# Optimization experiments

Measured on AMD Instinct MI355X. Metric: run time of the kernel, lower is better.

Reference implementation:

```python
import jax, jax.numpy as jnp
import numpy as np

N_ATOMS = 4096
HSIZE = 128
N_HEADS = 8
D_K = HSIZE // N_HEADS


def setup_inputs() -> dict:
    key = jax.random.key(0)
    ks = jax.random.split(key, 11)
    s = 1.0 / np.sqrt(HSIZE)
    return {
        "query": jax.random.normal(ks[0], (N_ATOMS, HSIZE), dtype=jnp.float32),
        "key": jax.random.normal(ks[1], (N_ATOMS, HSIZE), dtype=jnp.float32),
        "value": jax.random.normal(ks[2], (N_ATOMS, HSIZE), dtype=jnp.float32),
        "mask": jax.random.randint(ks[3], (N_ATOMS, N_ATOMS), 0, 2, dtype=jnp.int32),
        "Wq": jax.random.normal(ks[4], (HSIZE, HSIZE), dtype=jnp.float32) * s,
        "bq": jnp.zeros((HSIZE,), dtype=jnp.float32),
        "Wk": jax.random.normal(ks[5], (HSIZE, HSIZE), dtype=jnp.float32) * s,
        "bk": jnp.zeros((HSIZE,), dtype=jnp.float32),
        "Wv": jax.random.normal(ks[6], (HSIZE, HSIZE), dtype=jnp.float32) * s,
        "bv": jnp.zeros((HSIZE,), dtype=jnp.float32),
        "Wo": jax.random.normal(ks[7], (HSIZE, HSIZE), dtype=jnp.float32) * s,
    }


def _mha(query, key, value, mask, Wq, bq, Wk, bk, Wv, bv, Wo):
    n = query.shape[0]
    # project and split heads: [n, hsize] -> [H, n, d_k]
    def heads(x, W, b):
        return (x @ W.T + b).reshape(n, N_HEADS, D_K).transpose(1, 0, 2)
    q = heads(query, Wq, bq)
    k = heads(key, Wk, bk)
    v = heads(value, Wv, bv)
    scale = 1.0 / jnp.sqrt(jnp.asarray(D_K, q.dtype))
    scores = jnp.einsum("hnd,hmd->hnm", q, k) * scale  # [H, n, n]
    scores = jnp.where(mask[None, :, :] == 0, jnp.asarray(-1e9, scores.dtype), scores)
    p_attn = jax.nn.softmax(scores, axis=-1)
    x = jnp.einsum("hnm,hmd->hnd", p_attn, v)  # [H, n, d_k]
    x = x.transpose(1, 0, 2).reshape(n, HSIZE)  # merge heads
    return x @ Wo.T  # output_linear has bias=False


def reference(query, key, value, mask, Wq, bq, Wk, bk, Wv, bv, Wo):
    return _mha(query, key, value, mask, Wq, bq, Wk, bk, Wv, bv, Wo)
```

## Files before the change

### kernel.cpp

```cpp
#include <hip/hip_runtime.h>

#define NA 4096
#define HS 128
#define PSTR 72
#define CSTR 136

typedef unsigned short u16;
typedef unsigned long long u64;
using bf16x8  = __attribute__((ext_vector_type(8))) short;
using f32x4   = __attribute__((ext_vector_type(4))) float;
using ushort8 = __attribute__((ext_vector_type(8))) unsigned short;

#define QSCALE 0.18033688011112042f

static __device__ __forceinline__ u16 f2bf(float f) {
    unsigned u = __builtin_bit_cast(unsigned, f);
    u += 0x7FFFu + ((u >> 16) & 1u);
    return (u16)(u >> 16);
}

__global__ __launch_bounds__(256) void cvt_w(
    const float* __restrict__ Wq, const float* __restrict__ Wk,
    const float* __restrict__ Wv, const float* __restrict__ Wo,
    const float* __restrict__ bq, const float* __restrict__ bk,
    const float* __restrict__ bv,
    u16* __restrict__ Wf, float* __restrict__ bb)
{
    const int gid = blockIdx.x * 256 + threadIdx.x;
    const int e = gid * 4;
    const int mat = e >> 14, off = e & 16383;
    const float* src = (mat == 0) ? Wq : (mat == 1) ? Wk : (mat == 2) ? Wv : Wo;
    const float s = (mat == 0) ? QSCALE : 1.0f;
    float4 v = *(const float4*)(src + off);
    ushort4 o;
    o.x = f2bf(v.x * s); o.y = f2bf(v.y * s);
    o.z = f2bf(v.z * s); o.w = f2bf(v.w * s);
    const int j = off >> 7, k0 = off & 127;
    const int j0 = j >> 4, c = j & 15, kk = k0 >> 5, q = (k0 >> 3) & 3;
    const int tgt = mat * 16384 + ((j0 * 4 + kk) * 16 + c) * 32 + q * 8 + (k0 & 7);
    *(ushort4*)(Wf + tgt) = o;
    if (gid < 128)      bb[gid] = bq[gid] * QSCALE;
    else if (gid < 256) bb[gid] = bk[gid - 128];
    else if (gid < 384) bb[gid] = bv[gid - 256];
}

__global__ __launch_bounds__(256) void proj_mfma(
    const float* __restrict__ Xq, const float* __restrict__ Xk, const float* __restrict__ Xv,
    const u16* __restrict__ Wf, const float* __restrict__ bb,
    u16* __restrict__ Qbh, u16* __restrict__ Kbh, u16* __restrict__ VtB)
{
    const int mat = blockIdx.y;
    const float* X = (mat == 0) ? Xq : (mat == 1) ? Xk : Xv;
    const u16* Wm = Wf + mat * 16384;
    const float* bm = bb + mat * 128;
    const int r0b = blockIdx.x * 32;

    __shared__ __align__(16) u16 Xs[32 * CSTR];
    __shared__ __align__(16) u16 Cs[32 * CSTR];

    const int t = threadIdx.x;

    {
        const int r = t >> 3, cb = (t & 7) * 16;
        const float* Xr = X + (size_t)(r0b + r) * HS + cb;
#pragma unroll
        for (int seg = 0; seg < 4; ++seg) {
            float4 f = *(const float4*)(Xr + seg * 4);
            ushort4 u;
            u.x = f2bf(f.x); u.y = f2bf(f.y); u.z = f2bf(f.z); u.w = f2bf(f.w);
            *(ushort4*)(Xs + r * CSTR + cb + seg * 4) = u;
        }
    }
    __syncthreads();

    const int wv = t >> 6, lane = t & 63;
    const int c = lane & 15, q = lane >> 4;
    const int rw = (wv & 1) * 16;
    const int j0b = (wv >> 1) * 4;

    bf16x8 af[4];
#pragma unroll
    for (int kk = 0; kk < 4; ++kk)
        af[kk] = *(const bf16x8*)(Xs + (rw + c) * CSTR + kk * 32 + q * 8);

    const f32x4 zero = {0.f, 0.f, 0.f, 0.f};
#pragma unroll
    for (int jj = 0; jj < 4; ++jj) {
        const int j0 = j0b + jj;
        f32x4 acc = zero;
#pragma unroll
        for (int kk = 0; kk < 4; ++kk) {
            bf16x8 bf = *(const bf16x8*)(Wm + (j0 * 4 + kk) * 512 + c * 32 + q * 8);
            acc = __builtin_amdgcn_mfma_f32_16x16x32_bf16(af[kk], bf, acc, 0, 0, 0);
        }
        const float bias = bm[j0 * 16 + c];
#pragma unroll
        for (int r = 0; r < 4; ++r)
            Cs[(rw + 4 * q + r) * CSTR + j0 * 16 + c] = f2bf(acc[r] + bias);
    }
    __syncthreads();

    if (mat < 2) {
        u16* dst = (mat == 0) ? Qbh : Kbh;
        const int h8 = t >> 5, r = t & 31;
        const u16* src = Cs + r * CSTR + h8 * 16;
        u16* dp = dst + (size_t)h8 * (NA * 16) + (size_t)(r0b + r) * 16;
        *(bf16x8*)(dp)     = *(const bf16x8*)(src);
        *(bf16x8*)(dp + 8) = *(const bf16x8*)(src + 8);
    } else {
        const int d = t >> 1, s = t & 1;
        const int kb = r0b >> 6, ko = (r0b & 32) + s * 16;
        ushort8 v0, v1;
#pragma unroll
        for (int jj = 0; jj < 8; ++jj) v0[jj] = Cs[(s * 16 + jj) * CSTR + d];
#pragma unroll
        for (int jj = 0; jj < 8; ++jj) v1[jj] = Cs[(s * 16 + 8 + jj) * CSTR + d];
        u16* dp = VtB + (size_t)kb * 8192 + d * 64 + ko;
        *(ushort8*)(dp)     = v0;
        *(ushort8*)(dp + 8) = v1;
    }
}

__global__ __launch_bounds__(512, 8) void attn(
    const int* __restrict__ mask,
    const u16* __restrict__ Qbh, const u16* __restrict__ Kbh, const u16* __restrict__ VtB,
    float* __restrict__ part)
{
    __shared__ __align__(16) u16 Pbuf[8 * 16 * PSTR];
    __shared__ __align__(8)  u64 Mwp[16 * 17];

    const int t = threadIdx.x;
    const int h = t >> 6;
    const int lane = t & 63;
    const int c = lane & 15;
    const int q = lane >> 4;
    const int tile = blockIdx.x, split = blockIdx.y;
    const int i0 = tile * 16;
    const int kt0 = split * 1024;

#pragma unroll 4
    for (int rr = 0; rr < 32; ++rr) {
        const int idx = h * 32 + rr;
        const int row = idx >> 4, wc = idx & 15;
        const int v = mask[(size_t)(i0 + row) * NA + kt0 + wc * 64 + lane];
        u64 b = __ballot(v != 0);
        if (lane == 0) Mwp[row * 17 + wc] = b;
    }

    const u16* Qh = Qbh + (size_t)h * (NA * 16);
    const u16* Kh = Kbh + (size_t)h * (NA * 16);

    const bf16x8 qf = *(const bf16x8*)(Qh + (size_t)(i0 + c) * 16 + (q & 1) * 8);

    __syncthreads();

    const f32x4 zero = {0.f, 0.f, 0.f, 0.f};
    f32x4 Oacc = zero;
    float lsum = 0.f;
    u16* Pw = Pbuf + h * 16 * PSTR;

#pragma unroll 1
    for (int it = 0; it < 16; ++it) {
        const int kt = kt0 + it * 64;
        const u16* Vb = VtB + (size_t)(kt >> 6) * 8192 + (h * 16 + c) * 64;

        f32x4 ST[4];
#pragma unroll
        for (int t4 = 0; t4 < 4; ++t4) {
            bf16x8 kf = *(const bf16x8*)(Kh + (size_t)(kt + t4 * 16 + c) * 16 + (q & 1) * 8);
            ST[t4] = __builtin_amdgcn_mfma_f32_16x16x32_bf16(kf, qf, zero, 0, 0, 0);
        }
        bf16x8 vf0 = *(const bf16x8*)(Vb + q * 8);
        bf16x8 vf1 = *(const bf16x8*)(Vb + 32 + q * 8);

        u64 w = Mwp[c * 17 + it] >> (4 * q);
        unsigned mlo = (unsigned)w, mhi = (unsigned)(w >> 32);

#pragma unroll
        for (int t4 = 0; t4 < 4; ++t4) {
            const unsigned mw = (t4 < 2) ? mlo : mhi;
            const int sh = (t4 & 1) * 16;
            float p0 = ((mw >> (sh + 0)) & 1) ? __builtin_amdgcn_exp2f(ST[t4][0]) : 0.f;
            float p1 = ((mw >> (sh + 1)) & 1) ? __builtin_amdgcn_exp2f(ST[t4][1]) : 0.f;
            float p2 = ((mw >> (sh + 2)) & 1) ? __builtin_amdgcn_exp2f(ST[t4][2]) : 0.f;
            float p3 = ((mw >> (sh + 3)) & 1) ? __builtin_amdgcn_exp2f(ST[t4][3]) : 0.f;
            lsum += (p0 + p1) + (p2 + p3);
            unsigned lo = ((__builtin_bit_cast(unsigned, p0) + 0x8000u) >> 16)
                        | ((__builtin_bit_cast(unsigned, p1) + 0x8000u) & 0xFFFF0000u);
            unsigned hi = ((__builtin_bit_cast(unsigned, p2) + 0x8000u) >> 16)
                        | ((__builtin_bit_cast(unsigned, p3) + 0x8000u) & 0xFFFF0000u);
            *(uint2*)(Pw + c * PSTR + t4 * 16 + 4 * q) = make_uint2(lo, hi);
        }
        __asm__ volatile("" ::: "memory");
        __builtin_amdgcn_s_waitcnt(0xC07F);
        __asm__ volatile("" ::: "memory");

        bf16x8 pf0 = *(const bf16x8*)(Pw + c * PSTR + q * 8);
        bf16x8 pf1 = *(const bf16x8*)(Pw + c * PSTR + 32 + q * 8);
        Oacc = __builtin_amdgcn_mfma_f32_16x16x32_bf16(pf0, vf0, Oacc, 0, 0, 0);
        Oacc = __builtin_amdgcn_mfma_f32_16x16x32_bf16(pf1, vf1, Oacc, 0, 0, 0);
    }

    lsum += __shfl_xor(lsum, 16, 64);
    lsum += __shfl_xor(lsum, 32, 64);

    float* base = part + (size_t)((tile * 4 + split) * 8 + h) * 272;
#pragma unroll
    for (int r = 0; r < 4; ++r)
        base[(4 * q + r) * 16 + c] = Oacc[r];
    if (q == 0) base[256 + c] = lsum;
}

__global__ __launch_bounds__(256) void reduce_out(
    const float* __restrict__ part, const u16* __restrict__ Wf,
    float* __restrict__ out)
{
    __shared__ __align__(16) u16 xs[16 * CSTR];

    const int t = threadIdx.x;
    const int tile = blockIdx.x;
    const int i0 = tile * 16;
    const float* Pt = part + (size_t)tile * 4 * 8 * 272;

    {
        const int i = t >> 4, d = t & 15;
#pragma unroll
        for (int h = 0; h < 8; ++h) {
            float os = 0.f, ls = 0.f;
#pragma unroll
            for (int s = 0; s < 4; ++s) {
                const float* b = Pt + (size_t)(s * 8 + h) * 272;
                os += b[i * 16 + d];
                ls += b[256 + i];
            }
            xs[i * CSTR + h * 16 + d] = f2bf(os / ls);
        }
    }
    __syncthreads();

    const int wv = t >> 6, lane = t & 63;
    const int c = lane & 15, q = lane >> 4;
    const u16* WoB = Wf + 3 * 16384;

    bf16x8 af[4];
#pragma unroll
    for (int kk = 0; kk < 4; ++kk)
        af[kk] = *(const bf16x8*)(xs + c * CSTR + kk * 32 + q * 8);

    const f32x4 zero = {0.f, 0.f, 0.f, 0.f};
#pragma unroll
    for (int jj = 0; jj < 2; ++jj) {
        const int j0 = wv * 2 + jj;
        f32x4 acc = zero;
#pragma unroll
        for (int kk = 0; kk < 4; ++kk) {
            bf16x8 bf = *(const bf16x8*)(WoB + (j0 * 4 + kk) * 512 + c * 32 + q * 8);
            acc = __builtin_amdgcn_mfma_f32_16x16x32_bf16(af[kk], bf, acc, 0, 0, 0);
        }
#pragma unroll
        for (int r = 0; r < 4; ++r)
            out[(size_t)(i0 + 4 * q + r) * HS + j0 * 16 + c] = acc[r];
    }
}

extern "C" void kernel_launch(void* const* d_in, const int* in_sizes, int n_in,
                              void* d_out, int out_size, void* d_ws, size_t ws_size,
                              hipStream_t stream) {
    const float* query = (const float*)d_in[0];
    const float* key   = (const float*)d_in[1];
    const float* value = (const float*)d_in[2];
    const int*   mask  = (const int*)d_in[3];
    const float* Wq    = (const float*)d_in[4];
    const float* bq    = (const float*)d_in[5];
    const float* Wk    = (const float*)d_in[6];
    const float* bk    = (const float*)d_in[7];
    const float* Wv    = (const float*)d_in[8];
    const float* bv    = (const float*)d_in[9];
    const float* Wo    = (const float*)d_in[10];

    u16* Qbh = (u16*)d_ws;
    u16* Kbh = Qbh + (size_t)NA * HS;
    u16* VtB = Kbh + (size_t)NA * HS;
    u16* Wf  = VtB + (size_t)NA * HS;
    float* bb    = (float*)(Wf + 4 * 16384);
    float* partb = bb + 384;

    cvt_w<<<64, 256, 0, stream>>>(Wq, Wk, Wv, Wo, bq, bk, bv, Wf, bb);
    proj_mfma<<<dim3(128, 3), 256, 0, stream>>>(query, key, value, Wf, bb, Qbh, Kbh, VtB);
    attn<<<dim3(256, 4), 512, 0, stream>>>(mask, Qbh, Kbh, VtB, partb);
    reduce_out<<<256, 256, 0, stream>>>(partb, Wf, (float*)d_out);
}
```

Before: 185.3 us.

## Prefetch next K tile and mask word, double-buffer P in LDS

The attention loop now loads the next iteration's K fragments and mask word into registers while the current tile's scores are computed, giving software pipelining of global loads across iterations. The P staging buffer in LDS is double-buffered per wave, and P is packed to bf16 with the HIP intrinsic instead of manual rounding. The loop is unrolled by two. This adds register pressure and doubles the Pbuf LDS footprint, and the volatile LDS accesses may limit compiler scheduling.

```diff
diff --git a/kernel.cpp b/kernel.cpp
--- a/kernel.cpp
+++ b/kernel.cpp
@@ -1,9 +1,11 @@
 #include <hip/hip_runtime.h>
+#include <hip/hip_bf16.h>
 
 #define NA 4096
 #define HS 128
 #define PSTR 72
 #define CSTR 136
+#define MW 17
 
 typedef unsigned short u16;
 typedef unsigned long long u64;
@@ -17,6 +19,13 @@
     unsigned u = __builtin_bit_cast(unsigned, f);
     u += 0x7FFFu + ((u >> 16) & 1u);
     return (u16)(u >> 16);
+}
+
+static __device__ __forceinline__ unsigned pkbf(float a, float b) {
+    __hip_bfloat162 p = __float22bfloat162_rn(make_float2(a, b));
+    unsigned r;
+    __builtin_memcpy(&r, &p, 4);
+    return r;
 }
 
 __global__ __launch_bounds__(256) void cvt_w(
@@ -59,7 +68,6 @@
     __shared__ __align__(16) u16 Cs[32 * CSTR];
 
     const int t = threadIdx.x;
-
     {
         const int r = t >> 3, cb = (t & 7) * 16;
         const float* Xr = X + (size_t)(r0b + r) * HS + cb;
@@ -126,8 +134,8 @@
     const u16* __restrict__ Qbh, const u16* __restrict__ Kbh, const u16* __restrict__ VtB,
     float* __restrict__ part)
 {
-    __shared__ __align__(16) u16 Pbuf[8 * 16 * PSTR];
-    __shared__ __align__(8)  u64 Mwp[16 * 17];
+    __shared__ __align__(16) u16 Pbuf[8 * 2 * 16 * PSTR];
+    __shared__ __align__(8)  u64 Mwp[16 * MW];
 
     const int t = threadIdx.x;
     const int h = t >> 6;
@@ -144,12 +152,11 @@
         const int row = idx >> 4, wc = idx & 15;
         const int v = mask[(size_t)(i0 + row) * NA + kt0 + wc * 64 + lane];
         u64 b = __ballot(v != 0);
-        if (lane == 0) Mwp[row * 17 + wc] = b;
+        if (lane == 0) Mwp[row * MW + wc] = b;
     }
 
     const u16* Qh = Qbh + (size_t)h * (NA * 16);
     const u16* Kh = Kbh + (size_t)h * (NA * 16);
-
     const bf16x8 qf = *(const bf16x8*)(Qh + (size_t)(i0 + c) * 16 + (q & 1) * 8);
 
     __syncthreads();
@@ -157,24 +164,36 @@
     const f32x4 zero = {0.f, 0.f, 0.f, 0.f};
     f32x4 Oacc = zero;
     float lsum = 0.f;
-    u16* Pw = Pbuf + h * 16 * PSTR;
-
-#pragma unroll 1
+
+    bf16x8 kf[4];
+#pragma unroll
+    for (int t4 = 0; t4 < 4; ++t4)
+        kf[t4] = *(const bf16x8*)(Kh + (size_t)(kt0 + t4 * 16 + c) * 16 + (q & 1) * 8);
+    u64 wcur = Mwp[c * MW + 0];
+
+#pragma unroll 2
     for (int it = 0; it < 16; ++it) {
         const int kt = kt0 + it * 64;
+
+        f32x4 ST[4];
+#pragma unroll
+        for (int t4 = 0; t4 < 4; ++t4)
+            ST[t4] = __builtin_amdgcn_mfma_f32_16x16x32_bf16(kf[t4], qf, zero, 0, 0, 0);
+
         const u16* Vb = VtB + (size_t)(kt >> 6) * 8192 + (h * 16 + c) * 64;
-
-        f32x4 ST[4];
-#pragma unroll
-        for (int t4 = 0; t4 < 4; ++t4) {
-            bf16x8 kf = *(const bf16x8*)(Kh + (size_t)(kt + t4 * 16 + c) * 16 + (q & 1) * 8);
-            ST[t4] = __builtin_amdgcn_mfma_f32_16x16x32_bf16(kf, qf, zero, 0, 0, 0);
-        }
         bf16x8 vf0 = *(const bf16x8*)(Vb + q * 8);
         bf16x8 vf1 = *(const bf16x8*)(Vb + 32 + q * 8);
 
-        u64 w = Mwp[c * 17 + it] >> (4 * q);
-        unsigned mlo = (unsigned)w, mhi = (unsigned)(w >> 32);
+        const int itn = (it < 15) ? it + 1 : 0;
+        const int ktn = kt0 + itn * 64;
+#pragma unroll
+        for (int t4 = 0; t4 < 4; ++t4)
+            kf[t4] = *(const bf16x8*)(Kh + (size_t)(ktn + t4 * 16 + c) * 16 + (q & 1) * 8);
+        u64 w = wcur >> (4 * q);
+        wcur = Mwp[c * MW + itn];
+
+        const unsigned mlo = (unsigned)w, mhi = (unsigned)(w >> 32);
+        volatile u16* Pw = Pbuf + h * (2 * 16 * PSTR) + (it & 1) * (16 * PSTR);
 
 #pragma unroll
         for (int t4 = 0; t4 < 4; ++t4) {
@@ -185,18 +204,15 @@
             float p2 = ((mw >> (sh + 2)) & 1) ? __builtin_amdgcn_exp2f(ST[t4][2]) : 0.f;
             float p3 = ((mw >> (sh + 3)) & 1) ? __builtin_amdgcn_exp2f(ST[t4][3]) : 0.f;
             lsum += (p0 + p1) + (p2 + p3);
-            unsigned lo = ((__builtin_bit_cast(unsigned, p0) + 0x8000u) >> 16)
-                        | ((__builtin_bit_cast(unsigned, p1) + 0x8000u) & 0xFFFF0000u);
-            unsigned hi = ((__builtin_bit_cast(unsigned, p2) + 0x8000u) >> 16)
-                        | ((__builtin_bit_cast(unsigned, p3) + 0x8000u) & 0xFFFF0000u);
-            *(uint2*)(Pw + c * PSTR + t4 * 16 + 4 * q) = make_uint2(lo, hi);
-        }
-        __asm__ volatile("" ::: "memory");
+            const unsigned lo = pkbf(p0, p1);
+            const unsigned hi = pkbf(p2, p3);
+            *(volatile u64*)(Pw + c * PSTR + t4 * 16 + 4 * q) =
+                (u64)lo | ((u64)hi << 32);
+        }
         __builtin_amdgcn_s_waitcnt(0xC07F);
-        __asm__ volatile("" ::: "memory");
-
-        bf16x8 pf0 = *(const bf16x8*)(Pw + c * PSTR + q * 8);
-        bf16x8 pf1 = *(const bf16x8*)(Pw + c * PSTR + 32 + q * 8);
+
+        bf16x8 pf0 = *(volatile const bf16x8*)(Pw + c * PSTR + q * 8);
+        bf16x8 pf1 = *(volatile const bf16x8*)(Pw + c * PSTR + 32 + q * 8);
         Oacc = __builtin_amdgcn_mfma_f32_16x16x32_bf16(pf0, vf0, Oacc, 0, 0, 0);
         Oacc = __builtin_amdgcn_mfma_f32_16x16x32_bf16(pf1, vf1, Oacc, 0, 0, 0);
     }
```

Measured after the change: 259.5 us. 1.4x slower.
